# Optimization experiments

Measured on AMD Instinct MI355X. Metric: run time of the kernel, lower is better.

Reference implementation:

```python
import jax, jax.numpy as jnp
import numpy as np

B, S, D_IN, D_OUT, H = 2, 2048, 1024, 1024, 16
HD = D_OUT // H

def setup_inputs() -> dict:
    key = jax.random.key(0)
    ks = jax.random.split(key, 6)
    sc = 1.0 / np.sqrt(D_IN)
    return {
        "x": jax.random.normal(ks[0], (B, S, D_IN), dtype=jnp.float32),
        "Wq": jax.random.normal(ks[1], (D_IN, D_OUT), dtype=jnp.float32) * sc,
        "Wk": jax.random.normal(ks[2], (D_IN, D_OUT), dtype=jnp.float32) * sc,
        "Wv": jax.random.normal(ks[3], (D_IN, D_OUT), dtype=jnp.float32) * sc,
        "Wo": jax.random.normal(ks[4], (D_OUT, D_OUT), dtype=jnp.float32) * (1.0 / np.sqrt(D_OUT)),
        "bo": jax.random.normal(ks[5], (D_OUT,), dtype=jnp.float32) * 0.01,
    }

def reference(x, Wq, Wk, Wv, Wo, bo):
    b, n, _ = x.shape
    # QKV projections -> [b, h, n, hd]
    def split_heads(t):
        return t.reshape(b, n, H, HD).transpose(0, 2, 1, 3)
    q = split_heads(x @ Wq)
    k = split_heads(x @ Wk)
    v = split_heads(x @ Wv)
    scores = jnp.einsum("bhqd,bhkd->bhqk", q, k) / jnp.sqrt(jnp.float32(HD))
    causal = jnp.tril(jnp.ones((n, n), dtype=bool))  # True = keep
    scores = jnp.where(causal[None, None], scores, -jnp.inf)
    attn = jax.nn.softmax(scores, axis=-1)
    ctx = jnp.einsum("bhqk,bhkd->bhqd", attn, v)  # [b,h,n,hd]
    ctx = ctx.transpose(0, 2, 1, 3).reshape(b, n, D_OUT)
    return ctx @ Wo + bo
```

## Files before the change

kernel.cpp:

```cpp
#include <hip/hip_runtime.h>

#define B_  2
#define S_  2048
#define D_  1024
#define H_  16
#define HD_ 64
#define M_  (B_*S_)

typedef __bf16 bf16_t;
typedef __bf16 bf16x8 __attribute__((ext_vector_type(8)));
typedef float  f32x4  __attribute__((ext_vector_type(4)));
typedef short  s16x4  __attribute__((ext_vector_type(4)));

union U16x8 { uint4 u; bf16x8 v; };
union U16x4 { uint2 u; bf16_t e[4]; };
union U16x4s { uint2 u; s16x4 s; bf16_t e[4]; };

__device__ __forceinline__ bf16x8 ld_frag(const bf16_t* p) {
    U16x8 t; t.u = *(const uint4*)p; return t.v;
}

__device__ __forceinline__ void gload16(const bf16_t* g, bf16_t* l) {
    __builtin_amdgcn_global_load_lds(
        (const __attribute__((address_space(1))) unsigned int*)g,
        (__attribute__((address_space(3))) unsigned int*)l,
        16, 0, 0);
}

__global__ __launch_bounds__(256) void ingest(const float* __restrict__ w0,
                                              const float* __restrict__ w1,
                                              const float* __restrict__ w2,
                                              const float* __restrict__ w3,
                                              const float* __restrict__ xin,
                                              bf16_t* __restrict__ wtout,
                                              bf16_t* __restrict__ xout) {
    const int RC = 1024;
    int z = blockIdx.z;
    if (z == 4) {
        int bid = blockIdx.y * 32 + blockIdx.x;
        int t = threadIdx.y * 32 + threadIdx.x;
        int i = bid * 4096 + t * 16;
#pragma unroll
        for (int g = 0; g < 2; g++) {
            float4 a = *(const float4*)(xin + i + g * 8);
            float4 b = *(const float4*)(xin + i + g * 8 + 4);
            bf16_t o[8] = {(bf16_t)a.x, (bf16_t)a.y, (bf16_t)a.z, (bf16_t)a.w,
                           (bf16_t)b.x, (bf16_t)b.y, (bf16_t)b.z, (bf16_t)b.w};
            *(uint4*)(xout + i + g * 8) = *(uint4*)o;
        }
        return;
    }
    __shared__ bf16_t tile[32][33];
    const float* in = (z == 0) ? w0 : (z == 1) ? w1 : (z == 2) ? w2 : w3;
    bf16_t* out = wtout + (size_t)z * RC * RC;
    int c0 = blockIdx.x * 32, r0 = blockIdx.y * 32;
    int tx = threadIdx.x, ty = threadIdx.y;
#pragma unroll
    for (int i = 0; i < 32; i += 8)
        tile[ty + i][tx] = (bf16_t)in[(size_t)(r0 + ty + i) * RC + c0 + tx];
    __syncthreads();
#pragma unroll
    for (int i = 0; i < 32; i += 8)
        out[(size_t)(c0 + ty + i) * RC + r0 + tx] = tile[tx][ty + i];
}

#define STAGE_TILE(A_, Wt_, koff, buf)                                        \
    _Pragma("unroll") for (int c = 0; c < 4; c++) {                           \
        int rb = c * 32 + wid * 8;                                            \
        gload16(A_  + arow + (size_t)rb * K + (koff), (buf) + rb * 64);       \
        gload16(Wt_ + brow + (size_t)rb * K + (koff), (buf) + 8192 + rb * 64);\
    }

#define GEMM_CORE(A_, Wt_)                                                    \
    const int K = 1024;                                                       \
    __shared__ __align__(16) bf16_t smem[32768];                              \
    int t = threadIdx.x;                                                      \
    int wid = t >> 6, lane = t & 63, ln = lane & 15, quad = lane >> 4;        \
    int wm = (wid >> 1) * 64, wn = (wid & 1) * 64;                            \
    f32x4 zero = {0.f, 0.f, 0.f, 0.f};                                        \
    f32x4 acc[4][4];                                                          \
    _Pragma("unroll") for (int i = 0; i < 4; i++)                             \
        _Pragma("unroll") for (int j = 0; j < 4; j++) acc[i][j] = zero;       \
    int sr8 = lane >> 3;                                                      \
    int scs = (((lane & 7) ^ sr8) * 8);              \
    int swr = (ln & 7) * 8;                          \
    const size_t arow = (size_t)(m0 + sr8) * K + scs;                         \
    const size_t brow = (size_t)(n0 + sr8) * K + scs;                         \
    STAGE_TILE(A_, Wt_, 0, smem)                                              \
    STAGE_TILE(A_, Wt_, 64, smem + 16384)                                     \
    for (int it = 0; it < 16; it++) {                                         \
        if (it < 15) asm volatile("s_waitcnt vmcnt(8)" ::: "memory");         \
        else         asm volatile("s_waitcnt vmcnt(0)" ::: "memory");         \
        __builtin_amdgcn_sched_barrier(0);                                    \
        __builtin_amdgcn_s_barrier();                                         \
        bf16_t* a_lds = smem + (it & 1) * 16384;                              \
        bf16_t* b_lds = a_lds + 8192;                                         \
        _Pragma("unroll") for (int ks = 0; ks < 2; ks++) {                    \
            bf16x8 af[4], bfr[4];                                             \
            _Pragma("unroll") for (int i = 0; i < 4; i++)                     \
                af[i] = ld_frag(a_lds + (wm + i * 16 + ln) * 64 +             \
                                ((ks * 32 + quad * 8) ^ swr));                \
            _Pragma("unroll") for (int j = 0; j < 4; j++)                     \
                bfr[j] = ld_frag(b_lds + (wn + j * 16 + ln) * 64 +            \
                                 ((ks * 32 + quad * 8) ^ swr));               \
            _Pragma("unroll") for (int i = 0; i < 4; i++)                     \
                _Pragma("unroll") for (int j = 0; j < 4; j++)                 \
                    acc[i][j] = __builtin_amdgcn_mfma_f32_16x16x32_bf16(      \
                        af[i], bfr[j], acc[i][j], 0, 0, 0);                   \
        }                                                                     \
        asm volatile("s_waitcnt lgkmcnt(0)" ::: "memory");                    \
        __builtin_amdgcn_sched_barrier(0);                                    \
        __builtin_amdgcn_s_barrier();                                        \
        if (it < 14) {                                                        \
            int koff = (it + 2) * 64;                                         \
            bf16_t* bufn = smem + (it & 1) * 16384;                           \
            STAGE_TILE(A_, Wt_, koff, bufn)                                   \
        }                                                                     \
    }

__global__ __launch_bounds__(256) void gemm_qkv(const bf16_t* __restrict__ A,
                                                const bf16_t* __restrict__ wtbase,
                                                bf16_t* __restrict__ outbase) {
    int wsel = blockIdx.x >> 3;
    int n0 = (blockIdx.x & 7) * 128;
    int m0 = blockIdx.y * 128;
    const bf16_t* Wt = wtbase + (size_t)wsel * 1024 * 1024;
    bf16_t* out = outbase + (size_t)wsel * 4 * 1024 * 1024;

    GEMM_CORE(A, Wt)

    if (wsel < 2) {
#pragma unroll
        for (int i = 0; i < 4; i++)
#pragma unroll
            for (int j = 0; j < 4; j++) {
                int n = n0 + wn + j * 16 + ln;
                int h = n >> 6, hd = n & 63;
#pragma unroll
                for (int r = 0; r < 4; r++) {
                    int m = m0 + wm + i * 16 + quad * 4 + r;
                    int b = m >> 11, s = m & 2047;
                    out[(((size_t)(b * H_ + h) * S_ + s) * HD_) + hd] =
                        (bf16_t)acc[i][j][r];
                }
            }
    } else {
        bf16_t* tr = smem;
#pragma unroll
        for (int i = 0; i < 4; i++)
#pragma unroll
            for (int j = 0; j < 4; j++) {
                U16x4 pk;
#pragma unroll
                for (int r = 0; r < 4; r++) pk.e[r] = (bf16_t)acc[i][j][r];
                *(uint2*)(tr + (wn + j * 16 + ln) * 136 + wm + i * 16 + quad * 4) = pk.u;
            }
        __syncthreads();
        int row = t >> 1, half = t & 1;
        int n = n0 + row;
        int h = n >> 6, hd = n & 63;
        int b = m0 >> 11, s0 = (m0 & 2047) + half * 64;
        const bf16_t* src = tr + row * 136 + half * 64;
        bf16_t* dst = out + (((size_t)(b * H_ + h) * HD_ + hd) * S_) + s0;
#pragma unroll
        for (int u = 0; u < 8; u++)
            *(uint4*)(dst + u * 8) = *(const uint4*)(src + u * 8);
    }
}

__global__ __launch_bounds__(256) void gemm_out(const bf16_t* __restrict__ A,
                                                const bf16_t* __restrict__ Wt,
                                                float* __restrict__ out,
                                                const float* __restrict__ bias) {
    const int N = 1024;
    int n0 = blockIdx.x * 128;
    int m0 = blockIdx.y * 128;

    GEMM_CORE(A, Wt)

#pragma unroll
    for (int i = 0; i < 4; i++)
#pragma unroll
        for (int j = 0; j < 4; j++) {
            int n = n0 + wn + j * 16 + ln;
            float bv = bias[n];
#pragma unroll
            for (int r = 0; r < 4; r++) {
                int m = m0 + wm + i * 16 + quad * 4 + r;
                out[(size_t)m * N + n] = acc[i][j][r] + bv;
            }
        }
}

__global__ __launch_bounds__(256) void attn64(const bf16_t* __restrict__ Q,
                                              const bf16_t* __restrict__ Kg,
                                              const bf16_t* __restrict__ Vt,
                                              bf16_t* __restrict__ ctx) {
    __shared__ __align__(16) bf16_t k_lds[2][64 * 72];
    __shared__ __align__(16) bf16_t v_lds[2][64 * 76];

    int t = threadIdx.x;
    int wid = t >> 6, lane = t & 63, ln = lane & 15, quad = lane >> 4;

    int bid = blockIdx.x;
    int xcd = bid & 7;
    int c   = (bid >> 3) & 31;
    int g   = bid >> 8;
    int bh  = xcd + (g << 3);
    int qt  = (g & 1) ? c : (31 - c);
    int b = bh >> 4, h = bh & 15;
    const bf16_t* Qb = Q  + (size_t)bh * S_ * HD_;
    const bf16_t* Kb = Kg + (size_t)bh * S_ * HD_;
    const bf16_t* Vb = Vt + (size_t)bh * HD_ * S_;

    int srow = t >> 2, schunk = t & 3;
    f32x4 zero = {0.f, 0.f, 0.f, 0.f};

    int q0 = qt * 64;
    int nkt = qt + 1;

    int qrow = q0 + wid * 16 + ln;
    bf16x8 qf0 = ld_frag(Qb + (size_t)qrow * HD_ + quad * 8);
    bf16x8 qf1 = ld_frag(Qb + (size_t)qrow * HD_ + 32 + quad * 8);

    f32x4 oacc[4];
#pragma unroll
    for (int i = 0; i < 4; i++) oacc[i] = zero;
    float lsum = 0.f;

    {
        const uint4* ksrc = (const uint4*)(Kb + (size_t)srow * HD_);
        const uint4* vsrc = (const uint4*)(Vb + (size_t)srow * S_);
        uint4 kv0 = ksrc[schunk * 2], kv1 = ksrc[schunk * 2 + 1];
        uint4 vv0 = vsrc[schunk * 2], vv1 = vsrc[schunk * 2 + 1];
        *(uint4*)(k_lds[0] + srow * 72 + schunk * 16)     = kv0;
        *(uint4*)(k_lds[0] + srow * 72 + schunk * 16 + 8) = kv1;
        *(uint4*)(v_lds[0] + srow * 76 + schunk * 16)     = vv0;
        *(uint4*)(v_lds[0] + srow * 76 + schunk * 16 + 8) = vv1;
    }
    __syncthreads();

    for (int kt = 0; kt < nkt; kt++) {
        int cur = kt & 1;
        uint4 kv0, kv1, vv0, vv1;
        bool pf = (kt + 1 < nkt);
        if (pf) {
            int k0n = (kt + 1) * 64;
            const uint4* ksrc = (const uint4*)(Kb + (size_t)(k0n + srow) * HD_);
            const uint4* vsrc = (const uint4*)(Vb + (size_t)srow * S_ + k0n);
            kv0 = ksrc[schunk * 2]; kv1 = ksrc[schunk * 2 + 1];
            vv0 = vsrc[schunk * 2]; vv1 = vsrc[schunk * 2 + 1];
        }

        const bf16_t* kl = k_lds[cur];
        const bf16_t* vl = v_lds[cur];

        f32x4 sacc[4];
#pragma unroll
        for (int tt = 0; tt < 4; tt++) sacc[tt] = zero;
#pragma unroll
        for (int tt = 0; tt < 4; tt++) {
            bf16x8 a0 = ld_frag(kl + (tt * 16 + ln) * 72 + quad * 8);
            bf16x8 a1 = ld_frag(kl + (tt * 16 + ln) * 72 + 32 + quad * 8);
            sacc[tt] = __builtin_amdgcn_mfma_f32_16x16x32_bf16(a0, qf0, sacc[tt], 0, 0, 0);
            sacc[tt] = __builtin_amdgcn_mfma_f32_16x16x32_bf16(a1, qf1, sacc[tt], 0, 0, 0);
        }

        U16x4s pa[4];
        if (kt == nkt - 1) {
#pragma unroll
            for (int tt = 0; tt < 4; tt++) {
#pragma unroll
                for (int r = 0; r < 4; r++) {
                    int kg = kt * 64 + tt * 16 + quad * 4 + r;
                    float pv = __expf(__builtin_fmaf((float)sacc[tt][r], 0.125f, -16.0f));
                    if (kg > qrow) pv = 0.f;
                    lsum += pv;
                    pa[tt].e[r] = (bf16_t)pv;
                }
            }
        } else {
#pragma unroll
            for (int tt = 0; tt < 4; tt++) {
#pragma unroll
                for (int r = 0; r < 4; r++) {
                    float pv = __expf(__builtin_fmaf((float)sacc[tt][r], 0.125f, -16.0f));
                    lsum += pv;
                    pa[tt].e[r] = (bf16_t)pv;
                }
            }
        }

#pragma unroll
        for (int th = 0; th < 4; th++) {
#pragma unroll
            for (int tt = 0; tt < 4; tt++) {
                U16x4s vb;
                vb.u = *(const uint2*)(vl + (th * 16 + ln) * 76 +
                                       tt * 16 + quad * 4);
                oacc[th] = __builtin_amdgcn_mfma_f32_16x16x16bf16_1k(
                    pa[tt].s, vb.s, oacc[th], 0, 0, 0);
            }
        }

        if (pf) {
            bf16_t* kn = k_lds[cur ^ 1];
            bf16_t* vn = v_lds[cur ^ 1];
            *(uint4*)(kn + srow * 72 + schunk * 16)     = kv0;
            *(uint4*)(kn + srow * 72 + schunk * 16 + 8) = kv1;
            *(uint4*)(vn + srow * 76 + schunk * 16)     = vv0;
            *(uint4*)(vn + srow * 76 + schunk * 16 + 8) = vv1;
        }
        __syncthreads();
    }

    lsum += __shfl_xor(lsum, 16);
    lsum += __shfl_xor(lsum, 32);

#pragma unroll
    for (int r = 0; r < 4; r++) {
        int q = q0 + wid * 16 + quad * 4 + r;
        float inv = 1.f / __shfl(lsum, quad * 4 + r);
#pragma unroll
        for (int th = 0; th < 4; th++) {
            int hd = h * 64 + th * 16 + ln;
            ctx[((size_t)(b * S_ + q)) * D_ + hd] = (bf16_t)(oacc[th][r] * inv);
        }
    }
}

extern "C" void kernel_launch(void* const* d_in, const int* in_sizes, int n_in,
                              void* d_out, int out_size, void* d_ws, size_t ws_size,
                              hipStream_t stream) {
    const float* x  = (const float*)d_in[0];
    const float* bo = (const float*)d_in[5];
    float* out = (float*)d_out;

    bf16_t* ws = (bf16_t*)d_ws;
    const size_t MM = 1024 * 1024;
    bf16_t* xb  = ws;
    bf16_t* ctx = xb;
    bf16_t* wtq = xb + 4 * MM;
    bf16_t* wto = wtq + 3 * MM;
    bf16_t* qb  = wto + MM;
    bf16_t* kb  = qb + 4 * MM;
    bf16_t* vtb = kb + 4 * MM;

    ingest<<<dim3(32, 32, 5), dim3(32, 8, 1), 0, stream>>>(
        (const float*)d_in[1], (const float*)d_in[2],
        (const float*)d_in[3], (const float*)d_in[4], x, wtq, xb);

    gemm_qkv<<<dim3(24, 32, 1), 256, 0, stream>>>(xb, wtq, qb);

    attn64<<<1024, 256, 0, stream>>>(qb, kb, vtb, ctx);

    gemm_out<<<dim3(8, 32, 1), 256, 0, stream>>>(ctx, wto, out, bo);
}
```

Baseline: 194.7 us.

## Widen attention blocks to 128 query rows and pair complementary causal tiles

The attention kernel now runs 8 waves per block. Each block covers 128 query rows, so every K/V tile loaded into LDS serves twice as many queries. Each block handles two query tiles, qt and 15-qt, one after the other, so every block does the same total causal work. The grid is halved to 512 blocks of 512 threads and the per-wave mask test is generalised. In exchange, the lower waves compute fully masked products on the last key tile, and there is a larger block-wide barrier every iteration.

Result: slower. 201.8 us (+3.6%).

```diff
diff --git a/kernel.cpp b/kernel.cpp
--- a/kernel.cpp
+++ b/kernel.cpp
@@ -192,7 +192,7 @@
         }
 }
 
-__global__ __launch_bounds__(256) void attn64(const bf16_t* __restrict__ Q,
+__global__ __launch_bounds__(512) void attn64(const bf16_t* __restrict__ Q,
                                               const bf16_t* __restrict__ Kg,
                                               const bf16_t* __restrict__ Vt,
                                               bf16_t* __restrict__ ctx) {
@@ -203,128 +203,120 @@
     int wid = t >> 6, lane = t & 63, ln = lane & 15, quad = lane >> 4;
 
     int bid = blockIdx.x;
-    int xcd = bid & 7;
-    int c   = (bid >> 3) & 31;
-    int g   = bid >> 8;
-    int bh  = xcd + (g << 3);
-    int qt  = (g & 1) ? c : (31 - c);
+    int xcd = bid & 7, slot = bid >> 3;
+    int bh  = xcd + ((slot >> 4) << 3);
+    int pair = slot & 15;
     int b = bh >> 4, h = bh & 15;
     const bf16_t* Qb = Q  + (size_t)bh * S_ * HD_;
     const bf16_t* Kb = Kg + (size_t)bh * S_ * HD_;
     const bf16_t* Vb = Vt + (size_t)bh * HD_ * S_;
 
-    int srow = t >> 2, schunk = t & 3;
+    int srow = t >> 3, schunk = t & 7;
     f32x4 zero = {0.f, 0.f, 0.f, 0.f};
 
-    int q0 = qt * 64;
-    int nkt = qt + 1;
-
-    int qrow = q0 + wid * 16 + ln;
-    bf16x8 qf0 = ld_frag(Qb + (size_t)qrow * HD_ + quad * 8);
-    bf16x8 qf1 = ld_frag(Qb + (size_t)qrow * HD_ + 32 + quad * 8);
-
-    f32x4 oacc[4];
-#pragma unroll
-    for (int i = 0; i < 4; i++) oacc[i] = zero;
-    float lsum = 0.f;
-
-    {
-        const uint4* ksrc = (const uint4*)(Kb + (size_t)srow * HD_);
-        const uint4* vsrc = (const uint4*)(Vb + (size_t)srow * S_);
-        uint4 kv0 = ksrc[schunk * 2], kv1 = ksrc[schunk * 2 + 1];
-        uint4 vv0 = vsrc[schunk * 2], vv1 = vsrc[schunk * 2 + 1];
-        *(uint4*)(k_lds[0] + srow * 72 + schunk * 16)     = kv0;
-        *(uint4*)(k_lds[0] + srow * 72 + schunk * 16 + 8) = kv1;
-        *(uint4*)(v_lds[0] + srow * 76 + schunk * 16)     = vv0;
-        *(uint4*)(v_lds[0] + srow * 76 + schunk * 16 + 8) = vv1;
-    }
-    __syncthreads();
-
-    for (int kt = 0; kt < nkt; kt++) {
-        int cur = kt & 1;
-        uint4 kv0, kv1, vv0, vv1;
-        bool pf = (kt + 1 < nkt);
-        if (pf) {
-            int k0n = (kt + 1) * 64;
-            const uint4* ksrc = (const uint4*)(Kb + (size_t)(k0n + srow) * HD_);
-            const uint4* vsrc = (const uint4*)(Vb + (size_t)srow * S_ + k0n);
-            kv0 = ksrc[schunk * 2]; kv1 = ksrc[schunk * 2 + 1];
-            vv0 = vsrc[schunk * 2]; vv1 = vsrc[schunk * 2 + 1];
-        }
-
-        const bf16_t* kl = k_lds[cur];
-        const bf16_t* vl = v_lds[cur];
-
-        f32x4 sacc[4];
-#pragma unroll
-        for (int tt = 0; tt < 4; tt++) sacc[tt] = zero;
-#pragma unroll
-        for (int tt = 0; tt < 4; tt++) {
-            bf16x8 a0 = ld_frag(kl + (tt * 16 + ln) * 72 + quad * 8);
-            bf16x8 a1 = ld_frag(kl + (tt * 16 + ln) * 72 + 32 + quad * 8);
-            sacc[tt] = __builtin_amdgcn_mfma_f32_16x16x32_bf16(a0, qf0, sacc[tt], 0, 0, 0);
-            sacc[tt] = __builtin_amdgcn_mfma_f32_16x16x32_bf16(a1, qf1, sacc[tt], 0, 0, 0);
-        }
-
-        U16x4s pa[4];
-        if (kt == nkt - 1) {
+    for (int pass = 0; pass < 2; pass++) {
+        int qt = pass ? (15 - pair) : pair;
+        int q0 = qt * 128;
+        int nkt = 2 * qt + 2;
+
+        int qrow = q0 + wid * 16 + ln;
+        bf16x8 qf0 = ld_frag(Qb + (size_t)qrow * HD_ + quad * 8);
+        bf16x8 qf1 = ld_frag(Qb + (size_t)qrow * HD_ + 32 + quad * 8);
+
+        f32x4 oacc[4];
+#pragma unroll
+        for (int i = 0; i < 4; i++) oacc[i] = zero;
+        float lsum = 0.f;
+
+        {
+            uint4 kv = ((const uint4*)(Kb + (size_t)srow * HD_))[schunk];
+            uint4 vv = ((const uint4*)(Vb + (size_t)srow * S_))[schunk];
+            *(uint4*)(k_lds[0] + srow * 72 + schunk * 8) = kv;
+            *(uint4*)(v_lds[0] + srow * 76 + schunk * 8) = vv;
+        }
+        __syncthreads();
+
+        for (int kt = 0; kt < nkt; kt++) {
+            int cur = kt & 1;
+            uint4 kv, vv;
+            bool pf = (kt + 1 < nkt);
+            if (pf) {
+                int k0n = (kt + 1) * 64;
+                kv = ((const uint4*)(Kb + (size_t)(k0n + srow) * HD_))[schunk];
+                vv = ((const uint4*)(Vb + (size_t)srow * S_ + k0n))[schunk];
+            }
+
+            const bf16_t* kl = k_lds[cur];
+            const bf16_t* vl = v_lds[cur];
+
+            f32x4 sacc[4];
+#pragma unroll
+            for (int tt = 0; tt < 4; tt++) sacc[tt] = zero;
 #pragma unroll
             for (int tt = 0; tt < 4; tt++) {
-#pragma unroll
-                for (int r = 0; r < 4; r++) {
-                    int kg = kt * 64 + tt * 16 + quad * 4 + r;
-                    float pv = __expf(__builtin_fmaf((float)sacc[tt][r], 0.125f, -16.0f));
-                    if (kg > qrow) pv = 0.f;
-                    lsum += pv;
-                    pa[tt].e[r] = (bf16_t)pv;
+                bf16x8 a0 = ld_frag(kl + (tt * 16 + ln) * 72 + quad * 8);
+                bf16x8 a1 = ld_frag(kl + (tt * 16 + ln) * 72 + 32 + quad * 8);
+                sacc[tt] = __builtin_amdgcn_mfma_f32_16x16x32_bf16(a0, qf0, sacc[tt], 0, 0, 0);
+                sacc[tt] = __builtin_amdgcn_mfma_f32_16x16x32_bf16(a1, qf1, sacc[tt], 0, 0, 0);
+            }
+
+            U16x4s pa[4];
+            bool diag = (kt * 64 + 63 > q0 + wid * 16);
+            if (diag) {
+#pragma unroll
+                for (int tt = 0; tt < 4; tt++) {
+#pragma unroll
+                    for (int r = 0; r < 4; r++) {
+                        int kg = kt * 64 + tt * 16 + quad * 4 + r;
+                        float pv = __expf(__builtin_fmaf((float)sacc[tt][r], 0.125f, -16.0f));
+                        if (kg > qrow) pv = 0.f;
+                        lsum += pv;
+                        pa[tt].e[r] = (bf16_t)pv;
+                    }
                 }
-            }
-        } else {
-#pragma unroll
-            for (int tt = 0; tt < 4; tt++) {
-#pragma unroll
-                for (int r = 0; r < 4; r++) {
-                    float pv = __expf(__builtin_fmaf((float)sacc[tt][r], 0.125f, -16.0f));
-                    lsum += pv;
-                    pa[tt].e[r] = (bf16_t)pv;
+            } else {
+#pragma unroll
+                for (int tt = 0; tt < 4; tt++) {
+#pragma unroll
+                    for (int r = 0; r < 4; r++) {
+                        float pv = __expf(__builtin_fmaf((float)sacc[tt][r], 0.125f, -16.0f));
+                        lsum += pv;
+                        pa[tt].e[r] = (bf16_t)pv;
+                    }
                 }
             }
-        }
-
-#pragma unroll
-        for (int th = 0; th < 4; th++) {
-#pragma unroll
-            for (int tt = 0; tt < 4; tt++) {
-                U16x4s vb;
-                vb.u = *(const uint2*)(vl + (th * 16 + ln) * 76 +
-                                       tt * 16 + quad * 4);
-                oacc[th] = __builtin_amdgcn_mfma_f32_16x16x16bf16_1k(
-                    pa[tt].s, vb.s, oacc[th], 0, 0, 0);
-            }
-        }
-
-        if (pf) {
-            bf16_t* kn = k_lds[cur ^ 1];
-            bf16_t* vn = v_lds[cur ^ 1];
-            *(uint4*)(kn + srow * 72 + schunk * 16)     = kv0;
-            *(uint4*)(kn + srow * 72 + schunk * 16 + 8) = kv1;
-            *(uint4*)(vn + srow * 76 + schunk * 16)     = vv0;
-            *(uint4*)(vn + srow * 76 + schunk * 16 + 8) = vv1;
-        }
-        __syncthreads();
-    }
-
-    lsum += __shfl_xor(lsum, 16);
-    lsum += __shfl_xor(lsum, 32);
-
-#pragma unroll
-    for (int r = 0; r < 4; r++) {
-        int q = q0 + wid * 16 + quad * 4 + r;
-        float inv = 1.f / __shfl(lsum, quad * 4 + r);
-#pragma unroll
-        for (int th = 0; th < 4; th++) {
-            int hd = h * 64 + th * 16 + ln;
-            ctx[((size_t)(b * S_ + q)) * D_ + hd] = (bf16_t)(oacc[th][r] * inv);
+
+#pragma unroll
+            for (int th = 0; th < 4; th++) {
+#pragma unroll
+                for (int tt = 0; tt < 4; tt++) {
+                    U16x4s vb;
+                    vb.u = *(const uint2*)(vl + (th * 16 + ln) * 76 +
+                                           tt * 16 + quad * 4);
+                    oacc[th] = __builtin_amdgcn_mfma_f32_16x16x16bf16_1k(
+                        pa[tt].s, vb.s, oacc[th], 0, 0, 0);
+                }
+            }
+
+            if (pf) {
+                *(uint4*)(k_lds[cur ^ 1] + srow * 72 + schunk * 8) = kv;
+                *(uint4*)(v_lds[cur ^ 1] + srow * 76 + schunk * 8) = vv;
+            }
+            __syncthreads();
+        }
+
+        lsum += __shfl_xor(lsum, 16);
+        lsum += __shfl_xor(lsum, 32);
+
+#pragma unroll
+        for (int r = 0; r < 4; r++) {
+            int q = q0 + wid * 16 + quad * 4 + r;
+            float inv = 1.f / __shfl(lsum, quad * 4 + r);
+#pragma unroll
+            for (int th = 0; th < 4; th++) {
+                int hd = h * 64 + th * 16 + ln;
+                ctx[((size_t)(b * S_ + q)) * D_ + hd] = (bf16_t)(oacc[th][r] * inv);
+            }
         }
     }
 }
@@ -352,7 +344,7 @@
 
     gemm_qkv<<<dim3(24, 32, 1), 256, 0, stream>>>(xb, wtq, qb);
 
-    attn64<<<1024, 256, 0, stream>>>(qb, kb, vtb, ctx);
+    attn64<<<512, 512, 0, stream>>>(qb, kb, vtb, ctx);
 
     gemm_out<<<dim3(8, 32, 1), 256, 0, stream>>>(ctx, wto, out, bo);
 }
```
